# Kernel optimization log

Measured on AMD Instinct MI355X. Metric: run time of the kernel, lower is better.

The kernel has to match this reference:

```python
import jax, jax.numpy as jnp
import numpy as np

EPS = 1e-05
NEG = -1e9

def rotate_half(x):
    x1, x2 = jnp.split(x, 2, axis=-1)
    return jnp.concatenate([-x2, x1], axis=-1)

def rmsnorm(x, w):
    xf = x.astype(jnp.float32)
    n = xf * jax.lax.rsqrt(jnp.mean(xf * xf, axis=-1, keepdims=True) + EPS)
    return w * n.astype(x.dtype)

def setup_inputs() -> dict:
    key = jax.random.key(0)
    ks = jax.random.split(key, 12)
    B, S, H, NH, DH, FF = 1, 2048, 2048, 16, 128, 8192
    x = jax.random.normal(ks[0], (B, S, H), jnp.float32)
    # additive causal mask [1,1,S,S]
    causal = jnp.where(jnp.tril(jnp.ones((S, S), bool)), 0.0, NEG).astype(jnp.float32)
    attention_mask = causal[None, None]
    alibi = 0.1 * jax.random.normal(ks[1], (1, NH, S, S), jnp.float32)
    # rotary angles [S, DH]
    inv = 1.0 / (10000.0 ** (jnp.arange(0, DH, 2, dtype=jnp.float32) / DH))
    ang = jnp.arange(S, dtype=jnp.float32)[:, None] * inv[None, :]
    freqs = jnp.concatenate([ang, ang], axis=-1)  # [S, DH]
    sc = 1.0 / np.sqrt(H)
    wq = sc * jax.random.normal(ks[2], (H, H), jnp.float32)
    wk = sc * jax.random.normal(ks[3], (H, H), jnp.float32)
    wv = sc * jax.random.normal(ks[4], (H, H), jnp.float32)
    wo = sc * jax.random.normal(ks[5], (H, H), jnp.float32)
    w1 = sc * jax.random.normal(ks[6], (H, FF), jnp.float32)
    w3 = sc * jax.random.normal(ks[7], (H, FF), jnp.float32)
    w2 = (1.0 / np.sqrt(FF)) * jax.random.normal(ks[8], (FF, H), jnp.float32)
    attn_norm_w = jnp.ones((H,), jnp.float32)
    ffn_norm_w = jnp.ones((H,), jnp.float32)
    return dict(x=x, attention_mask=attention_mask, alibi=alibi, freqs=freqs,
                wq=wq, wk=wk, wv=wv, wo=wo, w1=w1, w2=w2, w3=w3,
                attn_norm_w=attn_norm_w, ffn_norm_w=ffn_norm_w)

def reference(x, attention_mask, alibi, freqs, wq, wk, wv, wo, w1, w2, w3,
              attn_norm_w, ffn_norm_w):
    B, S, H = x.shape
    NH = 16
    DH = H // NH
    nx = rmsnorm(x, attn_norm_w)
    # projections -> [B, NH, S, DH]
    def heads(y):
        return y.reshape(B, S, NH, DH).transpose(0, 2, 1, 3)
    q = heads(nx @ wq)
    k = heads(nx @ wk)
    v = heads(nx @ wv)
    cos, sin = jnp.cos(freqs), jnp.sin(freqs)  # [S, DH] broadcasts over B,NH
    q = q * cos + rotate_half(q) * sin
    k = k * cos + rotate_half(k) * sin
    scores = jnp.einsum('bhqd,bhkd->bhqk', q, k) / np.sqrt(DH)
    scores = scores + attention_mask + alibi
    attn = jax.nn.softmax(scores, axis=-1)
    out = jnp.einsum('bhqk,bhkd->bhqd', attn, v)
    out = out.transpose(0, 2, 1, 3).reshape(B, S, H)
    x = x + out @ wo
    nx = rmsnorm(x, ffn_norm_w)
    ff = (jax.nn.silu(nx @ w1) * (nx @ w3)) @ w2
    return x + ff
```

## Files before the change

kernel.cpp:

```cpp
#include <hip/hip_runtime.h>
#include <hip/hip_bf16.h>
#include <math.h>

typedef __bf16 bf16x8 __attribute__((ext_vector_type(8)));
typedef float  f32x4  __attribute__((ext_vector_type(4)));
typedef unsigned short u16x8 __attribute__((ext_vector_type(8)));
typedef unsigned short u16x4 __attribute__((ext_vector_type(4)));

#define DEV static __device__ __forceinline__

DEV void gload16(const void* g, void* l) {
  __builtin_amdgcn_global_load_lds((__attribute__((address_space(1))) void*)g,
                                   (__attribute__((address_space(3))) void*)l,
                                   16, 0, 0);
}

DEV float bf2f(unsigned short u) {
  unsigned v = ((unsigned)u) << 16;
  return __builtin_bit_cast(float, v);
}
DEV unsigned short f2bf(float f) {
  unsigned u = __builtin_bit_cast(unsigned, f);
  u = u + 0x7fffu + ((u >> 16) & 1u);
  return (unsigned short)(u >> 16);
}

__global__ __launch_bounds__(256) void rmsnorm_k(const float* __restrict__ x,
    const float* __restrict__ w, unsigned short* __restrict__ out, int H) {
  int row = blockIdx.x;
  const float4* xr = (const float4*)(x + (size_t)row * H);
  float4 a = xr[threadIdx.x * 2], b = xr[threadIdx.x * 2 + 1];
  float ss = a.x*a.x + a.y*a.y + a.z*a.z + a.w*a.w
           + b.x*b.x + b.y*b.y + b.z*b.z + b.w*b.w;
#pragma unroll
  for (int o = 32; o; o >>= 1) ss += __shfl_down(ss, o, 64);
  __shared__ float red[4];
  if ((threadIdx.x & 63) == 0) red[threadIdx.x >> 6] = ss;
  __syncthreads();
  float rs = rsqrtf((red[0] + red[1] + red[2] + red[3]) * (1.0f / 2048.0f) + 1e-5f);
  size_t base = (size_t)row * H + threadIdx.x * 8;
  const float* wv = w + threadIdx.x * 8;
  float vals[8] = {a.x, a.y, a.z, a.w, b.x, b.y, b.z, b.w};
  u16x8 o8;
#pragma unroll
  for (int i = 0; i < 8; ++i) o8[i] = f2bf(vals[i] * rs * wv[i]);
  *(u16x8*)(out + base) = o8;
}

__global__ __launch_bounds__(256) void wtrans64_k(const float* __restrict__ W,
    unsigned short* __restrict__ Wt, int R, int C, int ilv) {
  __shared__ unsigned short tile[64][68];
  const int c0 = blockIdx.x * 64, r0 = blockIdx.y * 64;
  const int t = threadIdx.x;
  const int lr = t >> 4, lc4 = (t & 15) * 4;
#pragma unroll
  for (int i = 0; i < 4; ++i) {
    float4 v = *(const float4*)&W[(size_t)(r0 + lr + i * 16) * C + c0 + lc4];
    u16x4 s4;
    s4[0] = f2bf(v.x); s4[1] = f2bf(v.y); s4[2] = f2bf(v.z); s4[3] = f2bf(v.w);
    *(u16x4*)&tile[lr + i * 16][lc4] = s4;
  }
  __syncthreads();
  const int oc = t >> 3, seg = (t & 7) * 8;
#pragma unroll
  for (int i = 0; i < 2; ++i) {
    int c = c0 + oc + i * 32;
    u16x8 o8;
#pragma unroll
    for (int j = 0; j < 8; ++j) o8[j] = tile[seg + j][oc + i * 32];
    size_t dstrow = (ilv < 0) ? (size_t)c
                              : (size_t)(c >> 4) * 32 + (c & 15) + ilv * 16;
    *(u16x8*)&Wt[dstrow * R + r0 + seg] = o8;
  }
}


#define STG_A(H, BUF, KC) do {                                                 \
    gload16(Asrc0 + (size_t)(H) * 128 * lda + (KC),                            \
            &lds[(BUF) * 16384 + (H) * 8192 + w * 1024]);                      \
    gload16(Asrc1 + (size_t)(H) * 128 * lda + (KC),                            \
            &lds[(BUF) * 16384 + (H) * 8192 + w * 1024 + 512]);                \
  } while (0)

#define STG_B(H, BUF, KC) do {                                                 \
    gload16(Bsrc0 + (size_t)(H) * 128 * ldb + (KC),                            \
            &lds[32768 + (BUF) * 16384 + (H) * 8192 + w * 1024]);              \
    gload16(Bsrc1 + (size_t)(H) * 128 * ldb + (KC),                            \
            &lds[32768 + (BUF) * 16384 + (H) * 8192 + w * 1024 + 512]);        \
  } while (0)

#define DS_A(DST, MH) do {                                                     \
    const int abase = buf * 16384 + (MH) * 8192 + arow * 64;                   \
    _Pragma("unroll") for (int m = 0; m < 4; ++m) {                            \
      DST[m][0] = *(const bf16x8*)&lds[abase + m * 1024 + acol0];              \
      DST[m][1] = *(const bf16x8*)&lds[abase + m * 1024 + acol1];              \
    } } while (0)

#define DS_B(DST, NH) do {                                                     \
    const int bbase = 32768 + buf * 16384 + (NH) * 8192 + brow * 64;           \
    _Pragma("unroll") for (int n = 0; n < 2; ++n) {                            \
      DST[n][0] = *(const bf16x8*)&lds[bbase + n * 1024 + acol0];              \
      DST[n][1] = *(const bf16x8*)&lds[bbase + n * 1024 + acol1];              \
    } } while (0)

#define MFMA16(AI, AR, BR) do {                                                \
    __builtin_amdgcn_s_setprio(1);                                             \
    _Pragma("unroll") for (int m = 0; m < 4; ++m)                              \
      _Pragma("unroll") for (int n = 0; n < 2; ++n) {                          \
        acc[AI][m][n] = __builtin_amdgcn_mfma_f32_16x16x32_bf16(               \
            AR[m][0], BR[n][0], acc[AI][m][n], 0, 0, 0);                       \
        acc[AI][m][n] = __builtin_amdgcn_mfma_f32_16x16x32_bf16(               \
            AR[m][1], BR[n][1], acc[AI][m][n], 0, 0, 0);                       \
      }                                                                        \
    __builtin_amdgcn_s_setprio(0);                                             \
  } while (0)

template <int EPI>
__global__ __launch_bounds__(512, 2) void gemm256_k(
    const unsigned short* __restrict__ A, int lda,
    const unsigned short* __restrict__ B, int ldb,
    unsigned short* __restrict__ Cb, float* __restrict__ Cf,
    int M, int N, int Kext) {
  __shared__ unsigned short lds[65536];
  const int t = threadIdx.x, w = t >> 6, lane = t & 63;
  const int nbm = M >> 8, nbn = N >> 8, nwg = nbm * nbn;
  int id = blockIdx.x;
  id = (id & 7) * (nwg >> 3) + (id >> 3);
  const int bm = id % nbm, bn = id / nbm;
  const size_t m0 = (size_t)bm << 8, n0 = (size_t)bn << 8;
  const int koff = blockIdx.y * Kext;
  const int NT = Kext >> 6;
  const int scol = ((lane & 7) ^ (lane >> 3)) * 8;
  const unsigned short* Asrc0 = A + (m0 + w * 16 + (lane >> 3)) * (size_t)lda + koff + scol;
  const unsigned short* Asrc1 = A + (m0 + w * 16 + 8 + (lane >> 3)) * (size_t)lda + koff + scol;
  const unsigned short* Bsrc0 = B + (n0 + w * 16 + (lane >> 3)) * (size_t)ldb + koff + scol;
  const unsigned short* Bsrc1 = B + (n0 + w * 16 + 8 + (lane >> 3)) * (size_t)ldb + koff + scol;
  const int arow = (w >> 2) * 64 + (lane & 15);
  const int brow = (w & 3) * 32 + (lane & 15);
  const int acol0 = ((lane >> 4) * 8) ^ ((lane & 7) << 3);
  const int acol1 = acol0 ^ 32;
  f32x4 acc[4][4][2] = {};
  bf16x8 Acur[4][2], B0r[2][2], B1r[2][2];
  STG_A(0, 0, 0); STG_B(0, 0, 0); STG_A(1, 0, 0); STG_B(1, 0, 0);
  STG_A(0, 1, 64); STG_B(0, 1, 64);
  asm volatile("s_waitcnt vmcnt(4)" ::: "memory");
  __builtin_amdgcn_s_barrier();
  for (int kt = 0; kt < NT; ++kt) {
    const int buf = kt & 1;
    const int kc1 = (kt + 1) * 64, kc2 = (kt + 2) * 64;
    const bool p1 = (kt + 1 < NT), p2 = (kt + 2 < NT);
    DS_A(Acur, 0); DS_B(B0r, 0);
    if (p1) STG_A(1, buf ^ 1, kc1);
    __builtin_amdgcn_sched_barrier(0);
    __builtin_amdgcn_s_barrier();
    MFMA16(0, Acur, B0r);
    __builtin_amdgcn_s_barrier();
    DS_B(B1r, 1);
    if (p1) STG_B(1, buf ^ 1, kc1);
    __builtin_amdgcn_sched_barrier(0);
    __builtin_amdgcn_s_barrier();
    MFMA16(1, Acur, B1r);
    __builtin_amdgcn_s_barrier();
    DS_A(Acur, 1);
    if (p2) STG_A(0, buf, kc2);
    __builtin_amdgcn_sched_barrier(0);
    __builtin_amdgcn_s_barrier();
    MFMA16(3, Acur, B1r);
    __builtin_amdgcn_s_barrier();
    if (p2) STG_B(0, buf, kc2);
    __builtin_amdgcn_sched_barrier(0);
    __builtin_amdgcn_s_barrier();
    MFMA16(2, Acur, B0r);
    if (p2) { asm volatile("s_waitcnt vmcnt(4)" ::: "memory"); }
    else    { asm volatile("s_waitcnt vmcnt(0)" ::: "memory"); }
    __builtin_amdgcn_s_barrier();
  }
#pragma unroll
  for (int Mh = 0; Mh < 2; ++Mh)
#pragma unroll
    for (int Nh = 0; Nh < 2; ++Nh)
#pragma unroll
      for (int m = 0; m < 4; ++m) {
        size_t gr = m0 + Mh * 128 + (w >> 2) * 64 + m * 16 + (lane >> 4) * 4;
        if constexpr (EPI == 2) {
          size_t gc = (n0 >> 1) + Nh * 64 + (w & 3) * 16 + (lane & 15);
          f32x4 v0 = acc[Mh * 2 + Nh][m][0];
          f32x4 v1 = acc[Mh * 2 + Nh][m][1];
#pragma unroll
          for (int j = 0; j < 4; ++j) {
            float s = v0[j] / (1.0f + __expf(-v0[j]));
            Cb[(gr + j) * (size_t)(N >> 1) + gc] = f2bf(s * v1[j]);
          }
        } else {
#pragma unroll
          for (int n = 0; n < 2; ++n) {
            size_t gc = n0 + Nh * 128 + (w & 3) * 32 + n * 16 + (lane & 15);
            f32x4 v = acc[Mh * 2 + Nh][m][n];
#pragma unroll
            for (int j = 0; j < 4; ++j) {
              size_t o = (gr + j) * (size_t)N + gc;
              if constexpr (EPI == 0) Cb[o] = f2bf(v[j]);
              else Cf[(size_t)blockIdx.y * M * N + o] = v[j];
            }
          }
        }
      }
}

template <int EPI>
__global__ __launch_bounds__(256) void gemm_bt_k(
    const unsigned short* __restrict__ A, const unsigned short* __restrict__ B,
    float* __restrict__ Cf, unsigned short* __restrict__ Cb,
    const float* __restrict__ resid, int M, int N, int K) {
  constexpr int BK = 64;
  __shared__ unsigned short lA[128 * BK];
  __shared__ unsigned short lB[128 * BK];
  const int t = threadIdx.x, wave = t >> 6, lane = t & 63;
  int nwg = gridDim.x * gridDim.y;
  int id = blockIdx.y * gridDim.x + blockIdx.x;
  id = (id & 7) * (nwg >> 3) + (id >> 3);
  const int m0 = (id % gridDim.x) * 128, n0 = (id / gridDim.x) * 128;
  const int wr = (wave >> 1) * 64, wc = (wave & 1) * 64;
  f32x4 acc[4][4] = {};
  const int sr = t >> 3;
  const int sc = ((t & 7) ^ (sr & 7)) * 8;
  const unsigned short* Ab = A + (size_t)(m0 + sr) * K + sc;
  const unsigned short* Bb = B + (size_t)(n0 + sr) * K + sc;
  unsigned short* lAw = &lA[(wave * 8) * BK];
  unsigned short* lBw = &lB[(wave * 8) * BK];
  const int row = lane & 15, kg = (lane >> 4) * 8, swz = (lane & 7) << 3;
  for (int k0 = 0; k0 < K; k0 += BK) {
#pragma unroll
    for (int it = 0; it < 4; ++it) {
      gload16(Ab + (size_t)it * 32 * K + k0, lAw + it * 32 * BK);
      gload16(Bb + (size_t)it * 32 * K + k0, lBw + it * 32 * BK);
    }
    asm volatile("s_waitcnt vmcnt(0)" ::: "memory");
    __syncthreads();
#pragma unroll
    for (int kk = 0; kk < 2; ++kk) {
      bf16x8 af[4], bfr[4];
#pragma unroll
      for (int m = 0; m < 4; ++m)
        af[m] = *(const bf16x8*)&lA[(wr + m * 16 + row) * BK + ((kk * 32 + kg) ^ swz)];
#pragma unroll
      for (int n = 0; n < 4; ++n)
        bfr[n] = *(const bf16x8*)&lB[(wc + n * 16 + row) * BK + ((kk * 32 + kg) ^ swz)];
#pragma unroll
      for (int m = 0; m < 4; ++m)
#pragma unroll
        for (int n = 0; n < 4; ++n)
          acc[m][n] = __builtin_amdgcn_mfma_f32_16x16x32_bf16(af[m], bfr[n], acc[m][n], 0, 0, 0);
    }
    __syncthreads();
  }
  const int cg = lane >> 4, col = lane & 15;
#pragma unroll
  for (int m = 0; m < 4; ++m)
#pragma unroll
    for (int n = 0; n < 4; ++n) {
      int rr = m0 + wr + m * 16 + cg * 4;
      int cc = n0 + wc + n * 16 + col;
#pragma unroll
      for (int j = 0; j < 4; ++j) {
        float v = acc[m][n][j];
        size_t o = (size_t)(rr + j) * N + cc;
        if constexpr (EPI == 2) Cf[o] = v + resid[o];
        else if constexpr (EPI == 1) Cf[o] = v;
        else Cb[o] = f2bf(v);
      }
    }
}

__global__ __launch_bounds__(256) void rope_k(const unsigned short* __restrict__ qkv,
    const float* __restrict__ freqs, unsigned short* __restrict__ Qr,
    unsigned short* __restrict__ Kr, int S) {
  int idx = blockIdx.x * 256 + threadIdx.x;
  int dp = idx & 63, h = (idx >> 6) & 15, s = idx >> 10;
  float ang = freqs[s * 128 + dp];
  float c, sn;
  sincosf(ang, &sn, &c);
  size_t rq = (size_t)s * 6144 + h * 128 + dp;
  float q1 = bf2f(qkv[rq]),        q2 = bf2f(qkv[rq + 64]);
  float k1 = bf2f(qkv[rq + 2048]), k2 = bf2f(qkv[rq + 2048 + 64]);
  size_t ob = ((size_t)h * S + s) * 128 + dp;
  Qr[ob]      = f2bf(q1 * c - q2 * sn);
  Qr[ob + 64] = f2bf(q2 * c + q1 * sn);
  Kr[ob]      = f2bf(k1 * c - k2 * sn);
  Kr[ob + 64] = f2bf(k2 * c + k1 * sn);
}

__global__ __launch_bounds__(256) void vtrans_k(const unsigned short* __restrict__ qkv,
    unsigned short* __restrict__ Vt, int S) {
  __shared__ unsigned short tile[32][33];
  int h = blockIdx.z;
  int s0 = blockIdx.x * 32, d0 = blockIdx.y * 32;
  int tx = threadIdx.x, ty = threadIdx.y;
#pragma unroll
  for (int i = 0; i < 4; ++i)
    tile[ty + i * 8][tx] = qkv[(size_t)(s0 + ty + i * 8) * 6144 + 4096 + h * 128 + d0 + tx];
  __syncthreads();
#pragma unroll
  for (int i = 0; i < 4; ++i)
    Vt[((size_t)h * 128 + d0 + ty + i * 8) * S + s0 + tx] = tile[tx][ty + i * 8];
}

#define STGKV(KT, BUF) do {                                                    \
    _Pragma("unroll") for (int it = 0; it < 4; ++it)                           \
      gload16(Kb + (size_t)((KT) * 64 + it * 16 + sr) * 128 + scw,             \
              &lds[(BUF) * 8192 + (it * 16 + wave * 4) * 128]);                \
    _Pragma("unroll") for (int it = 0; it < 4; ++it)                           \
      gload16(Vb + (size_t)(it * 32 + vr) * S + (KT) * 64 + vcw,               \
              &lds[16384 + (BUF) * 8192 + (it * 32 + wave * 8) * 64]);         \
  } while (0)

#define ATTN_TILE(CUR, NXT, KT) do {                                           \
    const int buf = (KT) & 1;                                                  \
    const bool p1 = ((KT) + 1 < ktiles);                                       \
    if (p1) {                                                                  \
      STGKV((KT) + 1, buf ^ 1);                                                \
      _Pragma("unroll") for (int q8 = 0; q8 < 16; ++q8)                        \
        NXT[q8] = albase[(size_t)(q8 & 3) * S + ((KT) + 1) * 64 + (q8 >> 2) * 16]; \
      asm volatile("s_waitcnt vmcnt(24)" ::: "memory");                        \
    } else {                                                                   \
      asm volatile("s_waitcnt vmcnt(0)" ::: "memory");                         \
    }                                                                          \
    __builtin_amdgcn_s_barrier();                                              \
    f32x4 sf[4] = {};                                                          \
    _Pragma("unroll") for (int ks = 0; ks < 4; ++ks)                           \
      _Pragma("unroll") for (int n = 0; n < 4; ++n) {                          \
        bf16x8 kf = *(const bf16x8*)&lds[buf * 8192 + (n * 16 + row) * 128 +   \
                                         ((ks * 32 + kg) ^ kswz)];             \
        sf[n] = __builtin_amdgcn_mfma_f32_16x16x32_bf16(qf[ks], kf, sf[n], 0, 0, 0); \
      }                                                                        \
    float pv[4][4];                                                            \
    float tmax[4] = {-1e30f, -1e30f, -1e30f, -1e30f};                          \
    _Pragma("unroll") for (int n = 0; n < 4; ++n) {                            \
      int k_abs = (KT) * 64 + n * 16 + col;                                    \
      _Pragma("unroll") for (int j = 0; j < 4; ++j) {                          \
        int q_abs = q0 + wave * 16 + cg * 4 + j;                               \
        float v = sf[n][j] * scale + CUR[n * 4 + j];                           \
        if (k_abs > q_abs) v = -1e30f;                                         \
        pv[n][j] = v;                                                          \
        tmax[j] = fmaxf(tmax[j], v);                                           \
      } }                                                                      \
    _Pragma("unroll") for (int o2 = 1; o2 < 16; o2 <<= 1)                      \
      _Pragma("unroll") for (int j = 0; j < 4; ++j)                            \
        tmax[j] = fmaxf(tmax[j], __shfl_xor(tmax[j], o2, 64));                 \
    float alpha[4], rsum[4] = {};                                              \
    _Pragma("unroll") for (int j = 0; j < 4; ++j) {                            \
      float mn = fmaxf(m_run[j], tmax[j]);                                     \
      alpha[j] = __expf(m_run[j] - mn);                                        \
      m_run[j] = mn;                                                           \
    }                                                                          \
    _Pragma("unroll") for (int n = 0; n < 4; ++n)                              \
      _Pragma("unroll") for (int j = 0; j < 4; ++j) {                          \
        float p = __expf(pv[n][j] - m_run[j]);                                 \
        pv[n][j] = p;                                                          \
        rsum[j] += p;                                                          \
      }                                                                        \
    _Pragma("unroll") for (int o2 = 1; o2 < 16; o2 <<= 1)                      \
      _Pragma("unroll") for (int j = 0; j < 4; ++j)                            \
        rsum[j] += __shfl_xor(rsum[j], o2, 64);                                \
    _Pragma("unroll") for (int j = 0; j < 4; ++j)                              \
      l_run[j] = l_run[j] * alpha[j] + rsum[j];                                \
    _Pragma("unroll") for (int nn = 0; nn < 8; ++nn)                           \
      _Pragma("unroll") for (int j = 0; j < 4; ++j) o[nn][j] *= alpha[j];      \
    _Pragma("unroll") for (int n = 0; n < 4; ++n)                              \
      _Pragma("unroll") for (int j = 0; j < 4; ++j) {                          \
        int pr = cg * 4 + j;                                                   \
        pw[pr * 64 + ((n * 16 + col) ^ ((pr & 7) << 3))] = f2bf(pv[n][j]);     \
      }                                                                        \
    asm volatile("s_waitcnt lgkmcnt(0)" ::: "memory");                         \
    __builtin_amdgcn_sched_barrier(0);                                         \
    _Pragma("unroll") for (int kk = 0; kk < 2; ++kk) {                         \
      bf16x8 pf = *(const bf16x8*)&pw[row * 64 + ((kk * 32 + kg) ^ kswz)];     \
      _Pragma("unroll") for (int nn = 0; nn < 8; ++nn) {                       \
        bf16x8 vf = *(const bf16x8*)&lds[16384 + buf * 8192 +                  \
                                         (nn * 16 + row) * 64 +                \
                                         ((kk * 32 + kg) ^ kswz)];             \
        o[nn] = __builtin_amdgcn_mfma_f32_16x16x32_bf16(pf, vf, o[nn], 0, 0, 0); \
      } }                                                                      \
    __builtin_amdgcn_s_barrier();                                              \
  } while (0)

__global__ __launch_bounds__(256) void attn_k(
    const unsigned short* __restrict__ Qr, const unsigned short* __restrict__ Kr,
    const unsigned short* __restrict__ Vt, const float* __restrict__ alibi,
    unsigned short* __restrict__ Ao, int S) {
  __shared__ unsigned short lds[36864];
  const int t = threadIdx.x, wave = t >> 6, lane = t & 63;
  const int h = blockIdx.y, nq = gridDim.x, bx = blockIdx.x;
  const int qt = (bx & 1) ? (nq - 1 - (bx >> 1)) : (bx >> 1);
  const int q0 = qt * 64;
  const int sr = t >> 4, scw = ((t & 15) ^ ((t >> 4) & 7)) * 8;
  const int vr = t >> 3, vcw = ((t & 7) ^ ((t >> 3) & 7)) * 8;
  const unsigned short* Kb = Kr + (size_t)h * S * 128;
  const unsigned short* Vb = Vt + (size_t)h * 128 * S;
  const int row = lane & 15, kg = (lane >> 4) * 8, cg = lane >> 4, col = lane & 15;
  const int kswz = (lane & 7) << 3;
  bf16x8 qf[4];
  const unsigned short* Qrow = Qr + ((size_t)h * S + q0 + wave * 16 + row) * 128;
#pragma unroll
  for (int ks = 0; ks < 4; ++ks) qf[ks] = *(const bf16x8*)&Qrow[ks * 32 + kg];
  f32x4 o[8] = {};
  float m_run[4] = {-1e30f, -1e30f, -1e30f, -1e30f};
  float l_run[4] = {};
  unsigned short* pw = &lds[32768 + wave * 1024];
  const float scale = 0.08838834764831843f;
  const int ktiles = qt + 1;
  const float* albase = alibi + (size_t)h * S * S +
                        ((size_t)q0 + wave * 16 + cg * 4) * S + col;
  float alA[16], alB[16];
  STGKV(0, 0);
#pragma unroll
  for (int q8 = 0; q8 < 16; ++q8)
    alA[q8] = albase[(size_t)(q8 & 3) * S + (q8 >> 2) * 16];
  for (int kt = 0; kt < ktiles; kt += 2) {
    ATTN_TILE(alA, alB, kt);
    if (kt + 1 < ktiles) ATTN_TILE(alB, alA, kt + 1);
  }
#pragma unroll
  for (int nn = 0; nn < 8; ++nn)
#pragma unroll
    for (int j = 0; j < 4; ++j) {
      int q_abs = q0 + wave * 16 + cg * 4 + j;
      Ao[(size_t)q_abs * 2048 + h * 128 + nn * 16 + col] = f2bf(o[nn][j] / l_run[j]);
    }
}

__global__ __launch_bounds__(256) void reduce4_k(const float* __restrict__ part,
    const float* __restrict__ resid, float* __restrict__ out, int n4, size_t mn) {
  int i = blockIdx.x * 256 + threadIdx.x;
  if (i >= n4) return;
  const float4* p = (const float4*)part;
  size_t q = mn >> 2;
  float4 a = ((const float4*)resid)[i];
  float4 s0 = p[i], s1 = p[i + q], s2 = p[i + 2 * q], s3 = p[i + 3 * q];
  float4 r;
  r.x = a.x + s0.x + s1.x + s2.x + s3.x;
  r.y = a.y + s0.y + s1.y + s2.y + s3.y;
  r.z = a.z + s0.z + s1.z + s2.z + s3.z;
  r.w = a.w + s0.w + s1.w + s2.w + s3.w;
  ((float4*)out)[i] = r;
}

extern "C" void kernel_launch(void* const* d_in, const int* in_sizes, int n_in,
                              void* d_out, int out_size, void* d_ws, size_t ws_size,
                              hipStream_t stream) {
  const int S = 2048, H = 2048, NH = 16, DH = 128, FF = 8192;
  const float* x     = (const float*)d_in[0];
  const float* alibi = (const float*)d_in[2];
  const float* freqs = (const float*)d_in[3];
  const float* wq    = (const float*)d_in[4];
  const float* wk    = (const float*)d_in[5];
  const float* wv    = (const float*)d_in[6];
  const float* wo    = (const float*)d_in[7];
  const float* w1    = (const float*)d_in[8];
  const float* w2    = (const float*)d_in[9];
  const float* w3    = (const float*)d_in[10];
  const float* anw   = (const float*)d_in[11];
  const float* fnw   = (const float*)d_in[12];
  float* out = (float*)d_out;

  char* ws = (char*)d_ws;
  size_t off = 0;
  auto alloc = [&](size_t n) { char* p = ws + off; off += (n + 255) & ~(size_t)255; return p; };
  unsigned short* qkvT = (unsigned short*)alloc((size_t)3 * H * H * 2);
  unsigned short* woT  = (unsigned short*)alloc((size_t)H * H * 2);
  unsigned short* w13T = (unsigned short*)alloc((size_t)2 * FF * H * 2);
  unsigned short* w2T  = (unsigned short*)alloc((size_t)H * FF * 2);
  float*          x2   = (float*)alloc((size_t)S * H * 4);
  unsigned short* nx2  = (unsigned short*)alloc((size_t)S * H * 2);
  unsigned short* gbuf = (unsigned short*)alloc((size_t)S * FF * 2);
  unsigned short* nx   = (unsigned short*)alloc((size_t)S * H * 2);
  unsigned short* qkvb = (unsigned short*)alloc((size_t)S * 3 * H * 2);
  unsigned short* Qr   = (unsigned short*)alloc((size_t)NH * S * DH * 2);
  unsigned short* Kr   = (unsigned short*)alloc((size_t)NH * S * DH * 2);
  unsigned short* Vt   = (unsigned short*)alloc((size_t)NH * DH * S * 2);
  unsigned short* attno= (unsigned short*)alloc((size_t)S * H * 2);
  float* part = (float*)ws;

  dim3 tb32(32, 8);
  wtrans64_k<<<dim3(32, 32), 256, 0, stream>>>(wq, qkvT, H, H, -1);
  wtrans64_k<<<dim3(32, 32), 256, 0, stream>>>(wk, qkvT + (size_t)H * H, H, H, -1);
  wtrans64_k<<<dim3(32, 32), 256, 0, stream>>>(wv, qkvT + (size_t)2 * H * H, H, H, -1);
  wtrans64_k<<<dim3(32, 32), 256, 0, stream>>>(wo, woT, H, H, -1);
  wtrans64_k<<<dim3(128, 32), 256, 0, stream>>>(w1, w13T, H, FF, 0);
  wtrans64_k<<<dim3(128, 32), 256, 0, stream>>>(w3, w13T, H, FF, 1);
  wtrans64_k<<<dim3(32, 128), 256, 0, stream>>>(w2, w2T, FF, H, -1);

  rmsnorm_k<<<S, 256, 0, stream>>>(x, anw, nx, H);
  gemm256_k<0><<<dim3(192, 1), 512, 0, stream>>>(nx, H, qkvT, H, qkvb, nullptr, S, 3 * H, H);
  rope_k<<<(S * NH * 64) / 256, 256, 0, stream>>>(qkvb, freqs, Qr, Kr, S);
  vtrans_k<<<dim3(S / 32, DH / 32, NH), tb32, 0, stream>>>(qkvb, Vt, S);
  attn_k<<<dim3(S / 64, NH), 256, 0, stream>>>(Qr, Kr, Vt, alibi, attno, S);
  gemm_bt_k<2><<<dim3(16, 16), 256, 0, stream>>>(attno, woT, x2, nullptr, x, S, H, H);
  rmsnorm_k<<<S, 256, 0, stream>>>(x2, fnw, nx2, H);
  gemm256_k<2><<<dim3(512, 1), 512, 0, stream>>>(nx2, H, w13T, H, gbuf, nullptr, S, 2 * FF, H);
  gemm256_k<1><<<dim3(64, 4), 512, 0, stream>>>(gbuf, FF, w2T, FF, nullptr, part, S, H, H);
  reduce4_k<<<4096, 256, 0, stream>>>(part, x2, out, S * H / 4, (size_t)S * H);
}
```

Measured before the change: 537.2 us.

## Switch 256x256 GEMM to 32x32x16 MFMA with new wave tiling and prefetch order

Rewrites the main 256-tile GEMM inner loop to use 32x32x16 bf16 MFMA instead of 16x16x32, with waves arranged 4x2 (32x64 per wave per quadrant) and a reordered quadrant and stage schedule that prefetches more of the next tile up front. The SwiGLU weight interleave is changed from 16-column to 32-column groups to match the new output layout, and the epilogue is rewritten for the 32x32 accumulator layout. The aim is fewer MFMA issues and LDS reads per flop and better operand reuse. It raises register pressure and changes the LDS access pattern and wait counts.

```diff
diff --git a/kernel.cpp b/kernel.cpp
--- a/kernel.cpp
+++ b/kernel.cpp
@@ -4,6 +4,7 @@
 
 typedef __bf16 bf16x8 __attribute__((ext_vector_type(8)));
 typedef float  f32x4  __attribute__((ext_vector_type(4)));
+typedef float  f32x16 __attribute__((ext_vector_type(16)));
 typedef unsigned short u16x8 __attribute__((ext_vector_type(8)));
 typedef unsigned short u16x4 __attribute__((ext_vector_type(4)));
 
@@ -69,7 +70,7 @@
 #pragma unroll
     for (int j = 0; j < 8; ++j) o8[j] = tile[seg + j][oc + i * 32];
     size_t dstrow = (ilv < 0) ? (size_t)c
-                              : (size_t)(c >> 4) * 32 + (c & 15) + ilv * 16;
+                              : (size_t)(c >> 5) * 64 + (c & 31) + ilv * 32;
     *(u16x8*)&Wt[dstrow * R + r0 + seg] = o8;
   }
 }
@@ -89,29 +90,26 @@
             &lds[32768 + (BUF) * 16384 + (H) * 8192 + w * 1024 + 512]);        \
   } while (0)
 
-#define DS_A(DST, MH) do {                                                     \
-    const int abase = buf * 16384 + (MH) * 8192 + arow * 64;                   \
-    _Pragma("unroll") for (int m = 0; m < 4; ++m) {                            \
-      DST[m][0] = *(const bf16x8*)&lds[abase + m * 1024 + acol0];              \
-      DST[m][1] = *(const bf16x8*)&lds[abase + m * 1024 + acol1];              \
+#define DS_A(MH) do {                                                          \
+    const int abase = buf * 16384 + (MH) * 8192 + (wm * 32 + lrow) * 64;       \
+    _Pragma("unroll") for (int s = 0; s < 4; ++s)                              \
+      Acur[s] = *(const bf16x8*)&lds[abase + ((s * 16 + lhalf * 8) ^ lswz)];   \
+  } while (0)
+
+#define DS_B(NH) do {                                                          \
+    _Pragma("unroll") for (int j = 0; j < 2; ++j) {                            \
+      const int bbase = 32768 + buf * 16384 + (NH) * 8192 +                    \
+                        (wn * 64 + j * 32 + lrow) * 64;                        \
+      _Pragma("unroll") for (int s = 0; s < 4; ++s)                            \
+        Bcur[j][s] = *(const bf16x8*)&lds[bbase + ((s * 16 + lhalf * 8) ^ lswz)]; \
     } } while (0)
 
-#define DS_B(DST, NH) do {                                                     \
-    const int bbase = 32768 + buf * 16384 + (NH) * 8192 + brow * 64;           \
-    _Pragma("unroll") for (int n = 0; n < 2; ++n) {                            \
-      DST[n][0] = *(const bf16x8*)&lds[bbase + n * 1024 + acol0];              \
-      DST[n][1] = *(const bf16x8*)&lds[bbase + n * 1024 + acol1];              \
-    } } while (0)
-
-#define MFMA16(AI, AR, BR) do {                                                \
+#define MFMA8(Q) do {                                                          \
     __builtin_amdgcn_s_setprio(1);                                             \
-    _Pragma("unroll") for (int m = 0; m < 4; ++m)                              \
-      _Pragma("unroll") for (int n = 0; n < 2; ++n) {                          \
-        acc[AI][m][n] = __builtin_amdgcn_mfma_f32_16x16x32_bf16(               \
-            AR[m][0], BR[n][0], acc[AI][m][n], 0, 0, 0);                       \
-        acc[AI][m][n] = __builtin_amdgcn_mfma_f32_16x16x32_bf16(               \
-            AR[m][1], BR[n][1], acc[AI][m][n], 0, 0, 0);                       \
-      }                                                                        \
+    _Pragma("unroll") for (int j = 0; j < 2; ++j)                              \
+      _Pragma("unroll") for (int s = 0; s < 4; ++s)                            \
+        acc[Q][j] = __builtin_amdgcn_mfma_f32_32x32x16_bf16(                   \
+            Acur[s], Bcur[j][s], acc[Q][j], 0, 0, 0);                          \
     __builtin_amdgcn_s_setprio(0);                                             \
   } while (0)
 
@@ -135,76 +133,75 @@
   const unsigned short* Asrc1 = A + (m0 + w * 16 + 8 + (lane >> 3)) * (size_t)lda + koff + scol;
   const unsigned short* Bsrc0 = B + (n0 + w * 16 + (lane >> 3)) * (size_t)ldb + koff + scol;
   const unsigned short* Bsrc1 = B + (n0 + w * 16 + 8 + (lane >> 3)) * (size_t)ldb + koff + scol;
-  const int arow = (w >> 2) * 64 + (lane & 15);
-  const int brow = (w & 3) * 32 + (lane & 15);
-  const int acol0 = ((lane >> 4) * 8) ^ ((lane & 7) << 3);
-  const int acol1 = acol0 ^ 32;
-  f32x4 acc[4][4][2] = {};
-  bf16x8 Acur[4][2], B0r[2][2], B1r[2][2];
+  const int wm = w >> 1, wn = w & 1;
+  const int lrow = lane & 31, lhalf = lane >> 5, lswz = (lane & 7) << 3;
+  f32x16 acc[4][2] = {};
+  bf16x8 Acur[4], Bcur[2][4];
   STG_A(0, 0, 0); STG_B(0, 0, 0); STG_A(1, 0, 0); STG_B(1, 0, 0);
-  STG_A(0, 1, 64); STG_B(0, 1, 64);
-  asm volatile("s_waitcnt vmcnt(4)" ::: "memory");
+  STG_B(0, 1, 64); STG_A(1, 1, 64); STG_B(1, 1, 64);
+  asm volatile("s_waitcnt vmcnt(6)" ::: "memory");
   __builtin_amdgcn_s_barrier();
   for (int kt = 0; kt < NT; ++kt) {
     const int buf = kt & 1;
     const int kc1 = (kt + 1) * 64, kc2 = (kt + 2) * 64;
     const bool p1 = (kt + 1 < NT), p2 = (kt + 2 < NT);
-    DS_A(Acur, 0); DS_B(B0r, 0);
-    if (p1) STG_A(1, buf ^ 1, kc1);
+    DS_A(0); DS_B(0);
+    if (p1) STG_A(0, buf ^ 1, kc1);
     __builtin_amdgcn_sched_barrier(0);
     __builtin_amdgcn_s_barrier();
-    MFMA16(0, Acur, B0r);
-    __builtin_amdgcn_s_barrier();
-    DS_B(B1r, 1);
-    if (p1) STG_B(1, buf ^ 1, kc1);
-    __builtin_amdgcn_sched_barrier(0);
-    __builtin_amdgcn_s_barrier();
-    MFMA16(1, Acur, B1r);
-    __builtin_amdgcn_s_barrier();
-    DS_A(Acur, 1);
-    if (p2) STG_A(0, buf, kc2);
-    __builtin_amdgcn_sched_barrier(0);
-    __builtin_amdgcn_s_barrier();
-    MFMA16(3, Acur, B1r);
-    __builtin_amdgcn_s_barrier();
+    MFMA8(0);
+    __builtin_amdgcn_s_barrier();
+    DS_A(1);
     if (p2) STG_B(0, buf, kc2);
     __builtin_amdgcn_sched_barrier(0);
     __builtin_amdgcn_s_barrier();
-    MFMA16(2, Acur, B0r);
-    if (p2) { asm volatile("s_waitcnt vmcnt(4)" ::: "memory"); }
-    else    { asm volatile("s_waitcnt vmcnt(0)" ::: "memory"); }
+    MFMA8(2);
+    __builtin_amdgcn_s_barrier();
+    DS_B(1);
+    if (p2) STG_A(1, buf, kc2);
+    __builtin_amdgcn_sched_barrier(0);
+    __builtin_amdgcn_s_barrier();
+    MFMA8(3);
+    __builtin_amdgcn_s_barrier();
+    DS_A(0);
+    if (p2) STG_B(1, buf, kc2);
+    __builtin_amdgcn_sched_barrier(0);
+    __builtin_amdgcn_s_barrier();
+    MFMA8(1);
+    if (p2)      { asm volatile("s_waitcnt vmcnt(6)" ::: "memory"); }
+    else         { asm volatile("s_waitcnt vmcnt(0)" ::: "memory"); }
     __builtin_amdgcn_s_barrier();
   }
 #pragma unroll
   for (int Mh = 0; Mh < 2; ++Mh)
 #pragma unroll
-    for (int Nh = 0; Nh < 2; ++Nh)
-#pragma unroll
-      for (int m = 0; m < 4; ++m) {
-        size_t gr = m0 + Mh * 128 + (w >> 2) * 64 + m * 16 + (lane >> 4) * 4;
-        if constexpr (EPI == 2) {
-          size_t gc = (n0 >> 1) + Nh * 64 + (w & 3) * 16 + (lane & 15);
-          f32x4 v0 = acc[Mh * 2 + Nh][m][0];
-          f32x4 v1 = acc[Mh * 2 + Nh][m][1];
-#pragma unroll
-          for (int j = 0; j < 4; ++j) {
-            float s = v0[j] / (1.0f + __expf(-v0[j]));
-            Cb[(gr + j) * (size_t)(N >> 1) + gc] = f2bf(s * v1[j]);
-          }
-        } else {
-#pragma unroll
-          for (int n = 0; n < 2; ++n) {
-            size_t gc = n0 + Nh * 128 + (w & 3) * 32 + n * 16 + (lane & 15);
-            f32x4 v = acc[Mh * 2 + Nh][m][n];
-#pragma unroll
-            for (int j = 0; j < 4; ++j) {
-              size_t o = (gr + j) * (size_t)N + gc;
-              if constexpr (EPI == 0) Cb[o] = f2bf(v[j]);
-              else Cf[(size_t)blockIdx.y * M * N + o] = v[j];
-            }
+    for (int Nh = 0; Nh < 2; ++Nh) {
+      const int q = Mh * 2 + Nh;
+      const size_t gr0 = m0 + Mh * 128 + wm * 32 + lhalf * 4;
+      if constexpr (EPI == 2) {
+        size_t gc = ((n0 + (size_t)Nh * 128 + wn * 64) >> 1) + lrow;
+        f32x16 v0 = acc[q][0], v1 = acc[q][1];
+#pragma unroll
+        for (int r = 0; r < 16; ++r) {
+          size_t row = gr0 + (r & 3) + 8 * (r >> 2);
+          float sg = v0[r] / (1.0f + __expf(-v0[r]));
+          Cb[row * (size_t)(N >> 1) + gc] = f2bf(sg * v1[r]);
+        }
+      } else {
+#pragma unroll
+        for (int j = 0; j < 2; ++j) {
+          size_t gc = n0 + Nh * 128 + wn * 64 + j * 32 + lrow;
+          f32x16 v = acc[q][j];
+#pragma unroll
+          for (int r = 0; r < 16; ++r) {
+            size_t row = gr0 + (r & 3) + 8 * (r >> 2);
+            size_t o = row * (size_t)N + gc;
+            if constexpr (EPI == 0) Cb[o] = f2bf(v[r]);
+            else Cf[(size_t)blockIdx.y * M * N + o] = v[r];
           }
         }
       }
+    }
 }
 
 template <int EPI>
```

After: 561.3 us. +4.5%, slower.
